# Performance work log

Measured on AMD Instinct MI355X. Metric: run time of the kernel, lower is better.

Reference implementation:

```python
import jax, jax.numpy as jnp
import numpy as np

H = 1024
NH = 16
HD = H // NH
EPS = 1e-5


def _layernorm(x, g, b):
    mu = jnp.mean(x, axis=-1, keepdims=True)
    var = jnp.mean((x - mu) ** 2, axis=-1, keepdims=True)
    return (x - mu) * jax.lax.rsqrt(var + EPS) * g + b


def setup_inputs() -> dict:
    key = jax.random.key(0)
    ks = jax.random.split(key, 12)
    s = lambda fan_in: 1.0 / np.sqrt(fan_in)
    x = jax.random.normal(ks[0], (2, 2048, H), dtype=jnp.float32)
    return {
        "x": x,
        "ln1_g": jnp.ones((H,), jnp.float32),
        "ln1_b": jnp.zeros((H,), jnp.float32),
        "W_qkv": jax.random.uniform(ks[1], (H, 3 * H), jnp.float32, -s(H), s(H)),
        "b_qkv": jax.random.uniform(ks[2], (3 * H,), jnp.float32, -s(H), s(H)),
        "W_out": jax.random.uniform(ks[3], (H, H), jnp.float32, -s(H), s(H)),
        "b_out": jax.random.uniform(ks[4], (H,), jnp.float32, -s(H), s(H)),
        "ln2_g": jnp.ones((H,), jnp.float32),
        "ln2_b": jnp.zeros((H,), jnp.float32),
        "W1": jax.random.uniform(ks[5], (H, 4 * H), jnp.float32, -s(H), s(H)),
        "b1": jax.random.uniform(ks[6], (4 * H,), jnp.float32, -s(H), s(H)),
        "W2": jax.random.uniform(ks[7], (4 * H, H), jnp.float32, -s(4 * H), s(4 * H)),
        "b2": jax.random.uniform(ks[8], (H,), jnp.float32, -s(4 * H), s(4 * H)),
    }


def reference(x, ln1_g, ln1_b, W_qkv, b_qkv, W_out, b_out, ln2_g, ln2_b, W1, b1, W2, b2):
    B, S, _ = x.shape
    residual = x
    h = _layernorm(x, ln1_g, ln1_b)
    qkv = h @ W_qkv + b_qkv                     # [B,S,3H]
    qkv = qkv.reshape(B, S, 3, NH, HD)
    q, k, v = qkv[:, :, 0], qkv[:, :, 1], qkv[:, :, 2]  # [B,S,NH,HD]
    scale = 1.0 / np.sqrt(HD)
    attn = jnp.einsum("bqhd,bkhd->bhqk", q, k) * scale  # [B,NH,S,S]
    attn = jax.nn.softmax(attn, axis=-1)
    out = jnp.einsum("bhqk,bkhd->bqhd", attn, v).reshape(B, S, H)
    x = residual + (out @ W_out + b_out)
    residual = x
    h = _layernorm(x, ln2_g, ln2_b)
    h = jax.nn.gelu(h @ W1 + b1, approximate=False) @ W2 + b2
    return residual + h
```

## Files before the change

kernel.cpp:

```cpp
#include <hip/hip_runtime.h>
#include <hip/hip_bf16.h>
#include <math.h>

#define HDIM 1024
#define SEQ  2048
#define BATCH 2
#define NHEAD 16
#define HEADD 64

typedef short bf16x8 __attribute__((ext_vector_type(8)));
typedef float f32x4  __attribute__((ext_vector_type(4)));
typedef unsigned short u16x8 __attribute__((ext_vector_type(8)));
typedef unsigned short u16x4 __attribute__((ext_vector_type(4)));

__device__ __forceinline__ unsigned short f2bf(float f) {
    unsigned u = __float_as_uint(f);
    unsigned r = (u + 0x7FFFu + ((u >> 16) & 1u)) >> 16;
    return (unsigned short)r;
}
__device__ __forceinline__ unsigned pk2bf(float lo, float hi) {
    __hip_bfloat162 h = __float22bfloat162_rn(float2{lo, hi});
    unsigned r;
    __builtin_memcpy(&r, &h, 4);
    return r;
}
__device__ __forceinline__ float fexp2(float x) {
#if __has_builtin(__builtin_amdgcn_exp2f)
    return __builtin_amdgcn_exp2f(x);
#else
    return exp2f(x);
#endif
}
__device__ __forceinline__ float frcp(float x) {
#if __has_builtin(__builtin_amdgcn_rcpf)
    return __builtin_amdgcn_rcpf(x);
#else
    return 1.0f / x;
#endif
}
__device__ __forceinline__ float erf_fast(float x) {
    float ax = fabsf(x);
    float t = frcp(fmaf(0.3275911f, ax, 1.0f));
    float p = fmaf(t, 1.061405429f, -1.453152027f);
    p = fmaf(p, t, 1.421413741f);
    p = fmaf(p, t, -0.284496736f);
    p = fmaf(p, t, 0.254829592f);
    p *= t;
    float e = fexp2(ax * ax * -1.4426950408889634f);
    return copysignf(fmaf(-p, e, 1.0f), x);
}
__device__ __forceinline__ float gelu_f(float v) {
    return 0.5f * v * (1.0f + erf_fast(v * 0.70710678118654752f));
}
__device__ __forceinline__ void gld16(void* lds, const void* g) {
    __builtin_amdgcn_global_load_lds(
        (const __attribute__((address_space(1))) unsigned int*)(g),
        (__attribute__((address_space(3))) unsigned int*)(lds),
        16, 0, 0);
}

#define SWZ(row, chunk) (((row) * 64) + (((chunk) ^ ((row) & 7)) << 3))

__global__ __launch_bounds__(256) void ln_kernel(const float* __restrict__ x,
                                                 const float* __restrict__ gw,
                                                 const float* __restrict__ bw,
                                                 unsigned short* __restrict__ y)
{
    int row = blockIdx.x;
    int t = threadIdx.x;
    const float* xr = x + (size_t)row * HDIM;
    float4 v = *(const float4*)(xr + t * 4);
    float s1 = v.x + v.y + v.z + v.w;
    float s2 = v.x * v.x + v.y * v.y + v.z * v.z + v.w * v.w;
#pragma unroll
    for (int m = 1; m < 64; m <<= 1) {
        s1 += __shfl_xor(s1, m);
        s2 += __shfl_xor(s2, m);
    }
    __shared__ float red[8];
    int wid = t >> 6;
    if ((t & 63) == 0) { red[wid * 2] = s1; red[wid * 2 + 1] = s2; }
    __syncthreads();
    if (t == 0) {
        float a = red[0] + red[2] + red[4] + red[6];
        float b = red[1] + red[3] + red[5] + red[7];
        red[0] = a; red[1] = b;
    }
    __syncthreads();
    float mu  = red[0] * (1.0f / HDIM);
    float var = red[1] * (1.0f / HDIM) - mu * mu;
    float rs  = rsqrtf(var + 1e-5f);
    float4 g4 = *(const float4*)(gw + t * 4);
    float4 b4 = *(const float4*)(bw + t * 4);
    ushort4 o;
    o.x = f2bf((v.x - mu) * rs * g4.x + b4.x);
    o.y = f2bf((v.y - mu) * rs * g4.y + b4.y);
    o.z = f2bf((v.z - mu) * rs * g4.z + b4.z);
    o.w = f2bf((v.w - mu) * rs * g4.w + b4.w);
    *(ushort4*)(y + (size_t)row * HDIM + t * 4) = o;
}

__global__ __launch_bounds__(256) void wconv_all(const float* __restrict__ Wq,
                                                 const float* __restrict__ Wo,
                                                 const float* __restrict__ W1,
                                                 const float* __restrict__ W2,
                                                 unsigned short* __restrict__ WqT,
                                                 unsigned short* __restrict__ WoT,
                                                 unsigned short* __restrict__ W1T,
                                                 unsigned short* __restrict__ W2T)
{
    int bid = blockIdx.x;
    const float* W; unsigned short* WT; int K, nx, idx;
    if (bid < 3072)      { W = Wq; WT = WqT; K = 1024; nx = 96;  idx = bid; }
    else if (bid < 4096) { W = Wo; WT = WoT; K = 1024; nx = 32;  idx = bid - 3072; }
    else if (bid < 8192) { W = W1; WT = W1T; K = 1024; nx = 128; idx = bid - 4096; }
    else                 { W = W2; WT = W2T; K = 4096; nx = 32;  idx = bid - 8192; }
    int N = nx * 32;
    int n0 = (idx % nx) * 32, k0 = (idx / nx) * 32;

    __shared__ float tile[32][33];
    int t = threadIdx.x, c = t & 31, r = t >> 5;
#pragma unroll
    for (int i = 0; i < 4; ++i)
        tile[r + 8 * i][c] = W[(size_t)(k0 + r + 8 * i) * N + n0 + c];
    __syncthreads();
#pragma unroll
    for (int i = 0; i < 4; ++i)
        WT[(size_t)(n0 + r + 8 * i) * K + k0 + c] = f2bf(tile[c][r + 8 * i]);
}

template <int EPI>
__global__ __launch_bounds__(256, 2) void mgemm(const unsigned short* __restrict__ A,
                                                const unsigned short* __restrict__ BT,
                                                const float* __restrict__ bias,
                                                const float* __restrict__ resid,
                                                float* __restrict__ Cf,
                                                unsigned short* __restrict__ Cb,
                                                int M, int N, int K)
{
    __shared__ char smem[65536];
    int t = threadIdx.x;
    int bn = blockIdx.x * 128, bm = blockIdx.y * 128;
    int l = t & 63, w = t >> 6;
    int wm = w >> 1, wn = w & 1;
    int lrow = l & 15, kq = l >> 4;

    f32x4 acc[4][4];
#pragma unroll
    for (int i = 0; i < 4; ++i)
#pragma unroll
        for (int j = 0; j < 4; ++j) acc[i][j] = {0.f, 0.f, 0.f, 0.f};

    const unsigned short* Ap[4];
    const unsigned short* Bp[4];
    int ld[4];
#pragma unroll
    for (int i = 0; i < 4; ++i) {
        int cid = i * 256 + t;
        int row = cid >> 3, c = cid & 7;
        int gc = (c ^ (row & 7)) << 3;
        Ap[i] = A + (size_t)(bm + row) * K + gc;
        int prow = (row & 64) + ((row & 15) << 2) + ((row >> 4) & 3);
        Bp[i] = BT + (size_t)(bn + prow) * K + gc;
        ld[i] = cid << 4;
    }

    int nt = K >> 6;
#pragma unroll
    for (int i = 0; i < 4; ++i) {
        gld16(smem + ld[i], Ap[i]);
        gld16(smem + 16384 + ld[i], Bp[i]);
    }
    __syncthreads();

    for (int tk = 0; tk < nt; ++tk) {
        int cur = (tk & 1) << 15;
        if (tk + 1 < nt) {
            int k0 = (tk + 1) << 6;
            int nxt = 32768 - cur;
#pragma unroll
            for (int i = 0; i < 4; ++i) {
                gld16(smem + nxt + ld[i], Ap[i] + k0);
                gld16(smem + nxt + 16384 + ld[i], Bp[i] + k0);
            }
        }
        const unsigned short* sA = (const unsigned short*)(smem + cur);
        const unsigned short* sB = (const unsigned short*)(smem + cur + 16384);
#pragma unroll
        for (int kk = 0; kk < 2; ++kk) {
            bf16x8 af[4], bv[4];
#pragma unroll
            for (int mi = 0; mi < 4; ++mi)
                af[mi] = *(const bf16x8*)(sA + SWZ(wm * 64 + mi * 16 + lrow, kk * 4 + kq));
#pragma unroll
            for (int ni = 0; ni < 4; ++ni)
                bv[ni] = *(const bf16x8*)(sB + SWZ(wn * 64 + ni * 16 + lrow, kk * 4 + kq));
#pragma unroll
            for (int mi = 0; mi < 4; ++mi)
#pragma unroll
                for (int ni = 0; ni < 4; ++ni)
                    acc[mi][ni] = __builtin_amdgcn_mfma_f32_16x16x32_bf16(af[mi], bv[ni], acc[mi][ni], 0, 0, 0);
        }
        __syncthreads();
    }

    int crow = (l >> 4) * 4;
    int ccol = l & 15;
    int gcolb = bn + wn * 64 + ccol * 4;
    float4 b4 = *(const float4*)(bias + gcolb);
#pragma unroll
    for (int mi = 0; mi < 4; ++mi) {
#pragma unroll
        for (int r = 0; r < 4; ++r) {
            int grow = bm + wm * 64 + mi * 16 + crow + r;
            size_t off = (size_t)grow * N + gcolb;
            float v0 = acc[mi][0][r] + b4.x;
            float v1 = acc[mi][1][r] + b4.y;
            float v2 = acc[mi][2][r] + b4.z;
            float v3 = acc[mi][3][r] + b4.w;
            if (EPI == 1) {
                float4 rr = *(const float4*)(resid + off);
                float4 o4 = {v0 + rr.x, v1 + rr.y, v2 + rr.z, v3 + rr.w};
                *(float4*)(Cf + off) = o4;
            } else {
                if (EPI == 2) {
                    v0 = gelu_f(v0); v1 = gelu_f(v1); v2 = gelu_f(v2); v3 = gelu_f(v3);
                }
                ushort4 o4 = {f2bf(v0), f2bf(v1), f2bf(v2), f2bf(v3)};
                *(ushort4*)(Cb + off) = o4;
            }
        }
    }
}

template <int EPI>
__global__ __launch_bounds__(256, 2) void mgemm64(const unsigned short* __restrict__ A,
                                                  const unsigned short* __restrict__ BT,
                                                  const float* __restrict__ bias,
                                                  const float* __restrict__ resid,
                                                  float* __restrict__ Cf,
                                                  unsigned short* __restrict__ Cb,
                                                  int M, int N, int K)
{
    __shared__ char smem[49152];
    int t = threadIdx.x;
    int bn = blockIdx.x * 128, bm = blockIdx.y * 64;
    int l = t & 63, w = t >> 6;
    int lrow = l & 15, kq = l >> 4;

    f32x4 acc[4][2];
#pragma unroll
    for (int i = 0; i < 4; ++i)
#pragma unroll
        for (int j = 0; j < 2; ++j) acc[i][j] = {0.f, 0.f, 0.f, 0.f};

    const unsigned short* Ap[2];
    int ldA[2];
#pragma unroll
    for (int i = 0; i < 2; ++i) {
        int cid = i * 256 + t;
        int row = cid >> 3, c = cid & 7;
        Ap[i] = A + (size_t)(bm + row) * K + ((c ^ (row & 7)) << 3);
        ldA[i] = cid << 4;
    }
    const unsigned short* Bp[4];
    int ldB[4];
#pragma unroll
    for (int i = 0; i < 4; ++i) {
        int cid = i * 256 + t;
        int row = cid >> 3, c = cid & 7;
        int prow = (row & ~31) + ((row & 15) << 1) + ((row >> 4) & 1);
        Bp[i] = BT + (size_t)(bn + prow) * K + ((c ^ (row & 7)) << 3);
        ldB[i] = cid << 4;
    }

    int nt = K >> 6;
#pragma unroll
    for (int i = 0; i < 2; ++i) gld16(smem + ldA[i], Ap[i]);
#pragma unroll
    for (int i = 0; i < 4; ++i) gld16(smem + 8192 + ldB[i], Bp[i]);
    __syncthreads();

    for (int tk = 0; tk < nt; ++tk) {
        int cur = (tk & 1) * 24576;
        if (tk + 1 < nt) {
            int k0 = (tk + 1) << 6;
            int nxt = 24576 - cur;
#pragma unroll
            for (int i = 0; i < 2; ++i) gld16(smem + nxt + ldA[i], Ap[i] + k0);
#pragma unroll
            for (int i = 0; i < 4; ++i) gld16(smem + nxt + 8192 + ldB[i], Bp[i] + k0);
        }
        const unsigned short* sA = (const unsigned short*)(smem + cur);
        const unsigned short* sB = (const unsigned short*)(smem + cur + 8192);
#pragma unroll
        for (int kk = 0; kk < 2; ++kk) {
            bf16x8 af[4], bv[2];
#pragma unroll
            for (int mi = 0; mi < 4; ++mi)
                af[mi] = *(const bf16x8*)(sA + SWZ(mi * 16 + lrow, kk * 4 + kq));
#pragma unroll
            for (int ni = 0; ni < 2; ++ni)
                bv[ni] = *(const bf16x8*)(sB + SWZ(w * 32 + ni * 16 + lrow, kk * 4 + kq));
#pragma unroll
            for (int mi = 0; mi < 4; ++mi)
#pragma unroll
                for (int ni = 0; ni < 2; ++ni)
                    acc[mi][ni] = __builtin_amdgcn_mfma_f32_16x16x32_bf16(af[mi], bv[ni], acc[mi][ni], 0, 0, 0);
        }
        __syncthreads();
    }

    int crow = (l >> 4) * 4;
    int ccol = l & 15;
    int gcolb = bn + w * 32 + ccol * 2;
    float2 b2 = *(const float2*)(bias + gcolb);
#pragma unroll
    for (int mi = 0; mi < 4; ++mi) {
#pragma unroll
        for (int r = 0; r < 4; ++r) {
            int grow = bm + mi * 16 + crow + r;
            size_t off = (size_t)grow * N + gcolb;
            float v0 = acc[mi][0][r] + b2.x;
            float v1 = acc[mi][1][r] + b2.y;
            if (EPI == 1) {
                float2 rr = *(const float2*)(resid + off);
                float2 o2 = {v0 + rr.x, v1 + rr.y};
                *(float2*)(Cf + off) = o2;
            } else {
                if (EPI == 2) { v0 = gelu_f(v0); v1 = gelu_f(v1); }
                *(unsigned*)(Cb + off) = pk2bf(v0, v1);
            }
        }
    }
}

__global__ __launch_bounds__(512) void mattn(const unsigned short* __restrict__ qkv,
                                             unsigned short* __restrict__ out)
{
    __shared__ unsigned short Qs[128 * 64];
    __shared__ unsigned short Ks[2][64 * 64];
    __shared__ unsigned short Vt[2][64 * 64];
    __shared__ unsigned short Ps[8 * 16 * 64];
    int t = threadIdx.x;
    int w = t >> 6, l = t & 63;
    int lr = l & 15, lh = l >> 4;
    int hwid = blockIdx.x + (blockIdx.y << 4) + (blockIdx.z << 8);
    int xcd = hwid & 7, slot = hwid >> 3;
    int pair = (xcd << 2) + (slot >> 4);
    int q0 = (slot & 15) * 128;
    int hh = pair & 15, b = pair >> 4;
    const unsigned short* Qg = qkv + (size_t)b * SEQ * 3072 + hh * 64;
    const unsigned short* Kg = Qg + 1024;
    const unsigned short* Vg = Qg + 2048;

#pragma unroll
    for (int i = 0; i < 2; ++i) {
        int chunkid = i * 512 + t;
        int row = chunkid >> 3, c = chunkid & 7;
        gld16(((char*)Qs) + chunkid * 16,
              Qg + (size_t)(q0 + row) * 3072 + ((c ^ (row & 7)) << 3));
    }

    int kr0 = t >> 3, kc0 = t & 7;
    const unsigned short* Kp0 = Kg + (size_t)kr0 * 3072 + kc0 * 8;
    int kd0 = SWZ(kr0, kc0);
    int vk = (t & 31) * 2;
    int vd0 = ((t >> 5) & 15) * 4;
    const unsigned short* Vp0 = Vg + (size_t)vk * 3072 + vd0;
    const unsigned short* Vp1 = Vp0 + 3072;

    u16x8 k0 = *(const u16x8*)Kp0;
    u16x4 v0 = *(const u16x4*)Vp0;
    u16x4 v1 = *(const u16x4*)Vp1;
    Kp0 += 64 * 3072; Vp0 += 64 * 3072; Vp1 += 64 * 3072;

    __syncthreads();
    bf16x8 qa[2];
#pragma unroll
    for (int ks = 0; ks < 2; ++ks)
        qa[ks] = *(const bf16x8*)(Qs + SWZ(w * 16 + lr, ks * 4 + lh));

    *(u16x8*)(Ks[0] + kd0) = k0;
#pragma unroll
    for (int j = 0; j < 4; ++j) {
        int d = vd0 + j;
        unsigned pack = (unsigned)(unsigned short)v0[j] | ((unsigned)(unsigned short)v1[j] << 16);
        *(unsigned*)(Vt[0] + SWZ(d, vk >> 3) + (vk & 7)) = pack;
    }
    k0 = *(const u16x8*)Kp0;
    v0 = *(const u16x4*)Vp0; v1 = *(const u16x4*)Vp1;
    Kp0 += 64 * 3072; Vp0 += 64 * 3072; Vp1 += 64 * 3072;
    asm volatile("s_waitcnt lgkmcnt(0)" ::: "memory");
    __builtin_amdgcn_s_barrier();

    f32x4 o[4];
#pragma unroll
    for (int i = 0; i < 4; ++i) o[i] = {0.f, 0.f, 0.f, 0.f};
    float mr = -3.0e38f, lsum = 0.f;
    unsigned short* Pw = Ps + w * (16 * 64);
    const float C = 0.18033688011112042f;

    const int nt = SEQ / 64;
    for (int tt = 0; tt < nt; ++tt) {
        const unsigned short* Kc = Ks[tt & 1];
        const unsigned short* Vc = Vt[tt & 1];

        f32x4 s[4];
#pragma unroll
        for (int ni = 0; ni < 4; ++ni) s[ni] = {0.f, 0.f, 0.f, 0.f};
#pragma unroll
        for (int ks = 0; ks < 2; ++ks) {
#pragma unroll
            for (int ni = 0; ni < 4; ++ni) {
                bf16x8 kb = *(const bf16x8*)(Kc + SWZ(ni * 16 + lr, ks * 4 + lh));
                s[ni] = __builtin_amdgcn_mfma_f32_16x16x32_bf16(kb, qa[ks], s[ni], 0, 0, 0);
            }
        }
        float mx = s[0][0];
#pragma unroll
        for (int ni = 0; ni < 4; ++ni)
#pragma unroll
            for (int r = 0; r < 4; ++r) mx = fmaxf(mx, s[ni][r]);
        mx = fmaxf(mx, __shfl_xor(mx, 16));
        mx = fmaxf(mx, __shfl_xor(mx, 32));
        if (__any(mx > mr + 64.0f)) {
            float mn = fmaxf(mr, mx);
            float corr = fexp2((mr - mn) * C);
            mr = mn;
            lsum *= corr;
            float cr[4];
#pragma unroll
            for (int r = 0; r < 4; ++r) cr[r] = __shfl(corr, lh * 4 + r, 16);
#pragma unroll
            for (int nd = 0; nd < 4; ++nd) {
                o[nd][0] *= cr[0]; o[nd][1] *= cr[1];
                o[nd][2] *= cr[2]; o[nd][3] *= cr[3];
            }
        }
        float mc = mr * C;
        float rsum = 0.f;
#pragma unroll
        for (int ni = 0; ni < 4; ++ni)
#pragma unroll
            for (int r = 0; r < 4; ++r) {
                float p = fexp2(fmaf(s[ni][r], C, -mc));
                s[ni][r] = p;
                rsum += p;
            }
        rsum += __shfl_xor(rsum, 16);
        rsum += __shfl_xor(rsum, 32);
        lsum += rsum;
#pragma unroll
        for (int ni = 0; ni < 4; ++ni)
#pragma unroll
            for (int rp = 0; rp < 2; ++rp) {
                int k = ni * 16 + lh * 4 + rp * 2;
                *(unsigned*)(Pw + SWZ(lr, k >> 3) + (k & 7)) =
                    pk2bf(s[ni][rp * 2], s[ni][rp * 2 + 1]);
            }
#pragma unroll
        for (int ks = 0; ks < 2; ++ks) {
            bf16x8 pa = *(const bf16x8*)(Pw + SWZ(lr, ks * 4 + lh));
#pragma unroll
            for (int nd = 0; nd < 4; ++nd) {
                bf16x8 vb = *(const bf16x8*)(Vc + SWZ(nd * 16 + lr, ks * 4 + lh));
                o[nd] = __builtin_amdgcn_mfma_f32_16x16x32_bf16(pa, vb, o[nd], 0, 0, 0);
            }
        }

        if (tt + 1 < nt) {
            int nb = (tt & 1) ^ 1;
            *(u16x8*)(Ks[nb] + kd0) = k0;
#pragma unroll
            for (int j = 0; j < 4; ++j) {
                int d = vd0 + j;
                unsigned pack = (unsigned)(unsigned short)v0[j] | ((unsigned)(unsigned short)v1[j] << 16);
                *(unsigned*)(Vt[nb] + SWZ(d, vk >> 3) + (vk & 7)) = pack;
            }
            if (tt + 2 < nt) {
                k0 = *(const u16x8*)Kp0;
                v0 = *(const u16x4*)Vp0; v1 = *(const u16x4*)Vp1;
                Kp0 += 64 * 3072; Vp0 += 64 * 3072; Vp1 += 64 * 3072;
            }
            asm volatile("s_waitcnt lgkmcnt(0)" ::: "memory");
            __builtin_amdgcn_s_barrier();
        }
    }
    float inv = 1.0f / lsum;
    float ir[4];
#pragma unroll
    for (int r = 0; r < 4; ++r) ir[r] = __shfl(inv, lh * 4 + r, 16);
#pragma unroll
    for (int r = 0; r < 4; ++r) {
        int q = q0 + w * 16 + lh * 4 + r;
#pragma unroll
        for (int nd = 0; nd < 4; ++nd) {
            int d = nd * 16 + lr;
            out[(size_t)((size_t)b * SEQ + q) * HDIM + hh * 64 + d] = f2bf(o[nd][r] * ir[r]);
        }
    }
}

extern "C" void kernel_launch(void* const* d_in, const int* in_sizes, int n_in,
                              void* d_out, int out_size, void* d_ws, size_t ws_size,
                              hipStream_t stream)
{
    const float* x     = (const float*)d_in[0];
    const float* ln1_g = (const float*)d_in[1];
    const float* ln1_b = (const float*)d_in[2];
    const float* W_qkv = (const float*)d_in[3];
    const float* b_qkv = (const float*)d_in[4];
    const float* W_out = (const float*)d_in[5];
    const float* b_out = (const float*)d_in[6];
    const float* ln2_g = (const float*)d_in[7];
    const float* ln2_b = (const float*)d_in[8];
    const float* W1    = (const float*)d_in[9];
    const float* b1    = (const float*)d_in[10];
    const float* W2    = (const float*)d_in[11];
    const float* b2    = (const float*)d_in[12];
    float* out = (float*)d_out;
    char* ws8  = (char*)d_ws;

    const int M = BATCH * SEQ;
    const size_t MB = 1048576;

    unsigned short* hbuf = (unsigned short*)(ws8);
    unsigned short* qkvb = (unsigned short*)(ws8 + 8 * MB);
    unsigned short* attb = (unsigned short*)(ws8 + 32 * MB);
    unsigned short* ffn1 = (unsigned short*)(ws8 + 8 * MB);
    unsigned short* WqT  = (unsigned short*)(ws8 + 40 * MB);
    unsigned short* WoT  = (unsigned short*)(ws8 + 46 * MB);
    unsigned short* W1T  = (unsigned short*)(ws8 + 48 * MB);
    unsigned short* W2T  = (unsigned short*)(ws8 + 56 * MB);

    wconv_all<<<12288, 256, 0, stream>>>(W_qkv, W_out, W1, W2, WqT, WoT, W1T, W2T);

    ln_kernel<<<M, 256, 0, stream>>>(x, ln1_g, ln1_b, hbuf);
    mgemm<0><<<dim3(3 * HDIM / 128, M / 128), 256, 0, stream>>>(hbuf, WqT, b_qkv, nullptr, nullptr, qkvb, M, 3 * HDIM, HDIM);
    mattn<<<dim3(SEQ / 128, NHEAD, BATCH), 512, 0, stream>>>(qkvb, attb);
    mgemm64<1><<<dim3(HDIM / 128, M / 64), 256, 0, stream>>>(attb, WoT, b_out, x, out, nullptr, M, HDIM, HDIM);
    ln_kernel<<<M, 256, 0, stream>>>(out, ln2_g, ln2_b, hbuf);
    mgemm<2><<<dim3(4 * HDIM / 128, M / 128), 256, 0, stream>>>(hbuf, W1T, b1, nullptr, nullptr, ffn1, M, 4 * HDIM, HDIM);
    mgemm64<1><<<dim3(HDIM / 128, M / 64), 256, 0, stream>>>(ffn1, W2T, b2, out, out, nullptr, M, HDIM, 4 * HDIM);
}
```

Measured before the change: 217.3 us.

## Add 256x256-tile 8-wave pipelined GEMM for FFN1 with GELU epilogue

```diff
diff --git a/kernel.cpp b/kernel.cpp
--- a/kernel.cpp
+++ b/kernel.cpp
@@ -331,6 +331,116 @@
                 if (EPI == 2) { v0 = gelu_f(v0); v1 = gelu_f(v1); }
                 *(unsigned*)(Cb + off) = pk2bf(v0, v1);
             }
+        }
+    }
+}
+
+template <int EPI>
+__global__ __launch_bounds__(512, 1) void mgemm8p(const unsigned short* __restrict__ A,
+                                                  const unsigned short* __restrict__ BT,
+                                                  const float* __restrict__ bias,
+                                                  unsigned short* __restrict__ Cb,
+                                                  int M, int N, int K)
+{
+    __shared__ char smem[131072];
+    int t = threadIdx.x;
+    int bn = blockIdx.x * 256, bm = blockIdx.y * 256;
+    int l = t & 63, w = t >> 6;
+    int lr = l & 15, kq = l >> 4;
+
+    f32x4 acc[16][2];
+#pragma unroll
+    for (int i = 0; i < 16; ++i)
+#pragma unroll
+        for (int j = 0; j < 2; ++j) acc[i][j] = {0.f, 0.f, 0.f, 0.f};
+
+    int r0 = t >> 3, c0 = t & 7;
+    int g0 = (c0 ^ (r0 & 7)) << 3;
+    const unsigned short* A0 = A + (size_t)(bm + r0) * K + g0;
+    const unsigned short* A1 = A + (size_t)(bm + 64 + r0) * K + g0;
+    const unsigned short* A2 = A + (size_t)(bm + 128 + r0) * K + g0;
+    const unsigned short* A3 = A + (size_t)(bm + 192 + r0) * K + g0;
+    int pr0 = (r0 & ~31) + ((r0 & 15) << 1) + ((r0 >> 4) & 1);
+    const unsigned short* B0 = BT + (size_t)(bn + pr0) * K + g0;
+    const unsigned short* B1 = BT + (size_t)(bn + 64 + pr0) * K + g0;
+    const unsigned short* B2 = BT + (size_t)(bn + 128 + pr0) * K + g0;
+    const unsigned short* B3 = BT + (size_t)(bn + 192 + pr0) * K + g0;
+    int d0 = t << 4, d1 = d0 + 8192;
+
+#define STG8(buf, h, tk) { \
+        size_t ko_ = (size_t)(tk) << 6; \
+        char* bb_ = smem + (buf) * 65536; \
+        if ((h) == 0)      { gld16(bb_ + 32768 + d0, B0 + ko_); gld16(bb_ + 32768 + d1, B1 + ko_); } \
+        else if ((h) == 1) { gld16(bb_ + 49152 + d0, B2 + ko_); gld16(bb_ + 49152 + d1, B3 + ko_); } \
+        else if ((h) == 2) { gld16(bb_ + d0, A0 + ko_);         gld16(bb_ + d1, A1 + ko_); } \
+        else               { gld16(bb_ + 16384 + d0, A2 + ko_); gld16(bb_ + 16384 + d1, A3 + ko_); } }
+
+    int nt = K >> 6;
+    STG8(0, 0, 0) STG8(0, 1, 0) STG8(0, 2, 0) STG8(0, 3, 0)
+    asm volatile("s_waitcnt vmcnt(2)" ::: "memory");
+    __builtin_amdgcn_s_barrier();
+
+    for (int tt = 0; tt < nt; ++tt) {
+        int cb = tt & 1, nb = cb ^ 1;
+        bool pre = (tt + 1 < nt);
+        const unsigned short* Ab = (const unsigned short*)(smem + cb * 65536);
+        const unsigned short* Bb = (const unsigned short*)(smem + cb * 65536 + 32768);
+        bf16x8 bfv[2][2];
+#pragma unroll
+        for (int p = 0; p < 4; ++p) {
+            bf16x8 af[4][2];
+#pragma unroll
+            for (int m2 = 0; m2 < 4; ++m2)
+#pragma unroll
+                for (int kk = 0; kk < 2; ++kk)
+                    af[m2][kk] = *(const bf16x8*)(Ab + SWZ((p * 4 + m2) * 16 + lr, kk * 4 + kq));
+            if (p == 0) {
+#pragma unroll
+                for (int ni = 0; ni < 2; ++ni)
+#pragma unroll
+                    for (int kk = 0; kk < 2; ++kk)
+                        bfv[ni][kk] = *(const bf16x8*)(Bb + SWZ(w * 32 + ni * 16 + lr, kk * 4 + kq));
+            }
+            if (pre) STG8(nb, p, tt + 1)
+            __builtin_amdgcn_s_barrier();
+            asm volatile("s_waitcnt lgkmcnt(0)" ::: "memory");
+            __builtin_amdgcn_sched_barrier(0);
+            __builtin_amdgcn_s_setprio(1);
+#pragma unroll
+            for (int m2 = 0; m2 < 4; ++m2)
+#pragma unroll
+                for (int ni = 0; ni < 2; ++ni)
+#pragma unroll
+                    for (int kk = 0; kk < 2; ++kk)
+                        acc[p * 4 + m2][ni] = __builtin_amdgcn_mfma_f32_16x16x32_bf16(
+                            af[m2][kk], bfv[ni][kk], acc[p * 4 + m2][ni], 0, 0, 0);
+            __builtin_amdgcn_s_setprio(0);
+            if (p == 1) {
+                if (pre) asm volatile("s_waitcnt vmcnt(4)" ::: "memory");
+                else     asm volatile("s_waitcnt vmcnt(0)" ::: "memory");
+            }
+            if (p == 3 && pre)
+                asm volatile("s_waitcnt vmcnt(2)" ::: "memory");
+            if (p < 3 || pre)
+                __builtin_amdgcn_s_barrier();
+        }
+    }
+#undef STG8
+
+    int crow = (l >> 4) * 4;
+    int ccol = l & 15;
+    int gcolb = bn + w * 32 + ccol * 2;
+    float2 b2 = *(const float2*)(bias + gcolb);
+#pragma unroll
+    for (int mi = 0; mi < 16; ++mi) {
+#pragma unroll
+        for (int r = 0; r < 4; ++r) {
+            int grow = bm + mi * 16 + crow + r;
+            size_t off = (size_t)grow * N + gcolb;
+            float v0 = acc[mi][0][r] + b2.x;
+            float v1 = acc[mi][1][r] + b2.y;
+            if (EPI == 2) { v0 = gelu_f(v0); v1 = gelu_f(v1); }
+            *(unsigned*)(Cb + off) = pk2bf(v0, v1);
         }
     }
 }
@@ -541,6 +651,6 @@
     mattn<<<dim3(SEQ / 128, NHEAD, BATCH), 512, 0, stream>>>(qkvb, attb);
     mgemm64<1><<<dim3(HDIM / 128, M / 64), 256, 0, stream>>>(attb, WoT, b_out, x, out, nullptr, M, HDIM, HDIM);
     ln_kernel<<<M, 256, 0, stream>>>(out, ln2_g, ln2_b, hbuf);
-    mgemm<2><<<dim3(4 * HDIM / 128, M / 128), 256, 0, stream>>>(hbuf, W1T, b1, nullptr, nullptr, ffn1, M, 4 * HDIM, HDIM);
+    mgemm8p<2><<<dim3(4 * HDIM / 256, M / 256), 512, 0, stream>>>(hbuf, W1T, b1, ffn1, M, 4 * HDIM, HDIM);
     mgemm64<1><<<dim3(HDIM / 128, M / 64), 256, 0, stream>>>(ffn1, W2T, b2, out, out, nullptr, M, HDIM, 4 * HDIM);
 }
```

Measured after the change: 218.3 us. Within noise of the previous version (+0.5%).
